# Optimization experiments

Hardware: AMD Instinct MI355X
Metric: run time of the kernel (lower is better)

The kernel has to match this reference:

```python
import jax, jax.numpy as jnp
import numpy as np

EMBED_DIM = 1024
NUM_HEADS = 16
HEAD_DIM = EMBED_DIM // NUM_HEADS


def layer_norm(x, gamma, beta, eps=1e-5):
    mu = jnp.mean(x, axis=-1, keepdims=True)
    var = jnp.var(x, axis=-1, keepdims=True)
    return (x - mu) * jax.lax.rsqrt(var + eps) * gamma + beta


def setup_inputs() -> dict:
    key = jax.random.key(0)
    ks = jax.random.split(key, 8)
    D = EMBED_DIM
    s = 1.0 / np.sqrt(D)
    x = jax.random.normal(ks[0], (2, 2048, D), dtype=jnp.float32)
    Wq = jax.random.uniform(ks[1], (D, D), jnp.float32, -s, s)
    Wk = jax.random.uniform(ks[2], (D, D), jnp.float32, -s, s)
    Wv = jax.random.uniform(ks[3], (D, D), jnp.float32, -s, s)
    W1 = jax.random.uniform(ks[4], (D, 4 * D), jnp.float32, -s, s)
    b1 = jnp.zeros((4 * D,), jnp.float32)
    W2 = jax.random.uniform(ks[5], (4 * D, D), jnp.float32, -1.0 / np.sqrt(4 * D), 1.0 / np.sqrt(4 * D))
    b2 = jnp.zeros((D,), jnp.float32)
    g1 = jnp.ones((D,), jnp.float32); be1 = jnp.zeros((D,), jnp.float32)
    g2 = jnp.ones((D,), jnp.float32); be2 = jnp.zeros((D,), jnp.float32)
    return {"x": x, "Wq": Wq, "Wk": Wk, "Wv": Wv, "W1": W1, "b1": b1,
            "W2": W2, "b2": b2, "g1": g1, "be1": be1, "g2": g2, "be2": be2}


def reference(x, Wq, Wk, Wv, W1, b1, W2, b2, g1, be1, g2, be2):
    B, S, D = x.shape
    H, Hd = NUM_HEADS, HEAD_DIM
    x_norm = layer_norm(x, g1, be1)
    # QKV projections (no bias), split into heads: [B, H, S, Hd]
    q = (x_norm @ Wq).reshape(B, S, H, Hd).transpose(0, 2, 1, 3)
    k = (x_norm @ Wk).reshape(B, S, H, Hd).transpose(0, 2, 1, 3)
    v = (x_norm @ Wv).reshape(B, S, H, Hd).transpose(0, 2, 1, 3)
    energy = jnp.einsum('bhqd,bhkd->bhqk', q, k)
    attn = jax.nn.softmax(energy / jnp.sqrt(jnp.float32(Hd)), axis=-1)
    out = jnp.einsum('bhqk,bhkd->bhqd', attn, v)
    attention = out.transpose(0, 2, 1, 3).reshape(B, S, D)
    x_res = attention + x
    x_norm2 = layer_norm(x_res, g2, be2)
    # Faithful quirk: FFN applied to x_res (not x_norm2)
    ffn_out = jax.nn.relu(x_res @ W1 + b1) @ W2 + b2
    return ffn_out + x_norm2
```

## Files before the change

kernel.cpp:

```cpp
#include <hip/hip_runtime.h>
#include <hip/hip_bf16.h>
#include <stdint.h>

typedef __hip_bfloat16 bf16;
typedef __attribute__((ext_vector_type(4))) float f32x4;
typedef __attribute__((ext_vector_type(8))) short s16x8;
typedef __attribute__((ext_vector_type(4))) short s16x4;

#define DEV static __device__ __forceinline__

DEV short f2bf(float f) {
  bf16 h = __float2bfloat16(f);
  short s;
  __builtin_memcpy(&s, &h, 2);
  return s;
}
DEV float bf2f(short s) {
  bf16 h;
  __builtin_memcpy(&h, &s, 2);
  return __bfloat162float(h);
}

__global__ __launch_bounds__(256) void transpose_cvt(
    const float* __restrict__ W, bf16* __restrict__ Wt, int K, int N)
{
  __shared__ float tile[32][33];
  const int n0 = blockIdx.x << 5;
  const int k0 = blockIdx.y << 5;
  const int tx = threadIdx.x & 31, ty = threadIdx.x >> 5;
#pragma unroll
  for (int i = 0; i < 4; ++i)
    tile[ty + i * 8][tx] = W[(size_t)(k0 + ty + i * 8) * N + n0 + tx];
  __syncthreads();
#pragma unroll
  for (int i = 0; i < 4; ++i)
    Wt[(size_t)(n0 + ty + i * 8) * K + k0 + tx] = __float2bfloat16(tile[tx][ty + i * 8]);
}

__global__ __launch_bounds__(256) void ln_bf16(
    const float* __restrict__ x, const float* __restrict__ g,
    const float* __restrict__ be, bf16* __restrict__ out)
{
  const int t = threadIdx.x;
  const size_t row = blockIdx.x;
  const float4 v = ((const float4*)(x + row * 1024))[t];
  float s = v.x + v.y + v.z + v.w;
  float ss = v.x * v.x + v.y * v.y + v.z * v.z + v.w * v.w;
#pragma unroll
  for (int off = 32; off > 0; off >>= 1) {
    s += __shfl_down(s, off);
    ss += __shfl_down(ss, off);
  }
  __shared__ float sh[8];
  const int wave = t >> 6, lane = t & 63;
  if (!lane) { sh[wave] = s; sh[4 + wave] = ss; }
  __syncthreads();
  s = sh[0] + sh[1] + sh[2] + sh[3];
  ss = sh[4] + sh[5] + sh[6] + sh[7];
  const float mean = s * (1.f / 1024.f);
  const float rstd = rsqrtf(ss * (1.f / 1024.f) - mean * mean + 1e-5f);
  const float4 gv = ((const float4*)g)[t];
  const float4 bv = ((const float4*)be)[t];
  s16x4 o;
  o[0] = f2bf((v.x - mean) * rstd * gv.x + bv.x);
  o[1] = f2bf((v.y - mean) * rstd * gv.y + bv.y);
  o[2] = f2bf((v.z - mean) * rstd * gv.z + bv.z);
  o[3] = f2bf((v.w - mean) * rstd * gv.w + bv.w);
  ((s16x4*)(out + row * 1024))[t] = o;
}

__global__ __launch_bounds__(256) void add_ln_bf16(
    const float* __restrict__ a, const float* __restrict__ x,
    const float* __restrict__ g, const float* __restrict__ be,
    bf16* __restrict__ xres, bf16* __restrict__ xnorm)
{
  const int t = threadIdx.x;
  const size_t row = blockIdx.x;
  const float4 av = ((const float4*)(a + row * 1024))[t];
  const float4 xv = ((const float4*)(x + row * 1024))[t];
  float4 v;
  v.x = av.x + xv.x; v.y = av.y + xv.y; v.z = av.z + xv.z; v.w = av.w + xv.w;
  float s = v.x + v.y + v.z + v.w;
  float ss = v.x * v.x + v.y * v.y + v.z * v.z + v.w * v.w;
#pragma unroll
  for (int off = 32; off > 0; off >>= 1) {
    s += __shfl_down(s, off);
    ss += __shfl_down(ss, off);
  }
  __shared__ float sh[8];
  const int wave = t >> 6, lane = t & 63;
  if (!lane) { sh[wave] = s; sh[4 + wave] = ss; }
  __syncthreads();
  s = sh[0] + sh[1] + sh[2] + sh[3];
  ss = sh[4] + sh[5] + sh[6] + sh[7];
  const float mean = s * (1.f / 1024.f);
  const float rstd = rsqrtf(ss * (1.f / 1024.f) - mean * mean + 1e-5f);
  const float4 gv = ((const float4*)g)[t];
  const float4 bv = ((const float4*)be)[t];
  s16x4 r, o;
  r[0] = f2bf(v.x); r[1] = f2bf(v.y); r[2] = f2bf(v.z); r[3] = f2bf(v.w);
  o[0] = f2bf((v.x - mean) * rstd * gv.x + bv.x);
  o[1] = f2bf((v.y - mean) * rstd * gv.y + bv.y);
  o[2] = f2bf((v.z - mean) * rstd * gv.z + bv.z);
  o[3] = f2bf((v.w - mean) * rstd * gv.w + bv.w);
  ((s16x4*)(xres + row * 1024))[t] = r;
  ((s16x4*)(xnorm + row * 1024))[t] = o;
}

template <int EPI>
__global__ __launch_bounds__(256) void gemm_bt(
    const bf16* __restrict__ A, const bf16* __restrict__ Bt,
    void* __restrict__ C, const float* __restrict__ bias,
    const bf16* __restrict__ add_bf16, int M, int N, int K)
{
  __shared__ bf16 sA0[128 * 64];
  __shared__ bf16 sB0[128 * 64];
  __shared__ bf16 sA1[128 * 64];
  __shared__ bf16 sB1[128 * 64];
  const int tid = threadIdx.x;
  const int wave = tid >> 6, lane = tid & 63;
  const int fr = lane & 15, fg = lane >> 4;
  const int f7 = fr & 7;
  const int wr = wave >> 1, wc = wave & 1;
  const int nbx = N >> 7;
  int bid = blockIdx.x;
  if ((gridDim.x & 7) == 0) {
    const int cpx = gridDim.x >> 3;
    bid = (bid & 7) * cpx + (bid >> 3);
  }
  const int brow = (bid / nbx) << 7;
  const int bcol = (bid % nbx) << 7;

  f32x4 acc[4][4] = {};

  const int rsub = lane >> 3;
  const int cl = (lane & 7) ^ rsub;
  size_t ga[4], gb[4];
  int la[4];
#pragma unroll
  for (int j = 0; j < 4; ++j) {
    const int r = wave * 32 + j * 8;
    ga[j] = (size_t)(brow + r + rsub) * K + cl * 8;
    gb[j] = (size_t)(bcol + r + rsub) * K + cl * 8;
    la[j] = r * 64;
  }

#define GSTAGE(SA, SB, koff)                                                   \
  do {                                                                         \
    _Pragma("unroll")                                                          \
    for (int jj = 0; jj < 4; ++jj) {                                           \
      __builtin_amdgcn_global_load_lds(                                        \
          (const __attribute__((address_space(1))) uint32_t*)(A + ga[jj] + (koff)), \
          (__attribute__((address_space(3))) uint32_t*)(&SA[la[jj]]), 16, 0, 0);  \
      __builtin_amdgcn_global_load_lds(                                        \
          (const __attribute__((address_space(1))) uint32_t*)(Bt + gb[jj] + (koff)),\
          (__attribute__((address_space(3))) uint32_t*)(&SB[la[jj]]), 16, 0, 0);  \
    }                                                                          \
  } while (0)

#define COMPUTE(SA, SB)                                                        \
  do {                                                                         \
    s16x8 af[4][2], bfr[4][2];                                                 \
    _Pragma("unroll")                                                          \
    for (int m = 0; m < 4; ++m)                                                \
      _Pragma("unroll")                                                        \
      for (int kk = 0; kk < 2; ++kk)                                           \
        af[m][kk] = *(const s16x8*)(&SA[(wr * 64 + m * 16 + fr) * 64 +         \
                                        (((kk * 4 + fg) ^ f7) << 3)]);         \
    _Pragma("unroll")                                                          \
    for (int n = 0; n < 4; ++n)                                                \
      _Pragma("unroll")                                                        \
      for (int kk = 0; kk < 2; ++kk)                                           \
        bfr[n][kk] = *(const s16x8*)(&SB[(wc * 64 + n * 16 + fr) * 64 +        \
                                         (((kk * 4 + fg) ^ f7) << 3)]);        \
    _Pragma("unroll")                                                          \
    for (int kk = 0; kk < 2; ++kk)                                             \
      _Pragma("unroll")                                                        \
      for (int m = 0; m < 4; ++m)                                              \
        _Pragma("unroll")                                                      \
        for (int n = 0; n < 4; ++n)                                            \
          acc[m][n] = __builtin_amdgcn_mfma_f32_16x16x32_bf16(                 \
              af[m][kk], bfr[n][kk], acc[m][n], 0, 0, 0);                      \
  } while (0)

  GSTAGE(sA0, sB0, 0);
  __syncthreads();

  int kt = 0;
  for (;;) {
    if (kt + 64 < K) {
      GSTAGE(sA1, sB1, kt + 64);
      COMPUTE(sA0, sB0);
      __syncthreads();
    } else {
      COMPUTE(sA0, sB0);
      break;
    }
    kt += 64;
    if (kt + 64 < K) {
      GSTAGE(sA0, sB0, kt + 64);
      COMPUTE(sA1, sB1);
      __syncthreads();
    } else {
      COMPUTE(sA1, sB1);
      break;
    }
    kt += 64;
  }
#undef GSTAGE
#undef COMPUTE

  const int crow = brow + wr * 64;
  const int ccol = bcol + wc * 64;
#pragma unroll
  for (int m = 0; m < 4; ++m) {
#pragma unroll
    for (int n = 0; n < 4; ++n) {
      const int col = ccol + n * 16 + fr;
#pragma unroll
      for (int j = 0; j < 4; ++j) {
        const int row = crow + m * 16 + fg * 4 + j;
        float v = acc[m][n][j];
        if (EPI == 0) {
          ((bf16*)C)[(size_t)row * N + col] = __float2bfloat16(v);
        } else if (EPI == 1) {
          v += bias[col];
          v = fmaxf(v, 0.f);
          ((bf16*)C)[(size_t)row * N + col] = __float2bfloat16(v);
        } else {
          float a;
          {
            bf16 hb = add_bf16[(size_t)row * N + col];
            a = __bfloat162float(hb);
          }
          ((float*)C)[(size_t)row * N + col] = v + bias[col] + a;
        }
      }
    }
  }
}

template <int EPI>
__global__ __launch_bounds__(512) void gemm256_bt(
    const bf16* __restrict__ A, const bf16* __restrict__ Bt,
    void* __restrict__ C, const float* __restrict__ bias, int M, int N, int K)
{
  __shared__ bf16 sA0[256 * 64];
  __shared__ bf16 sB0[256 * 64];
  __shared__ bf16 sA1[256 * 64];
  __shared__ bf16 sB1[256 * 64];
  const int tid = threadIdx.x;
  const int wave = tid >> 6, lane = tid & 63;
  const int fr = lane & 15, fg = lane >> 4;
  const int f7 = fr & 7;
  const int wr = wave >> 2, wc = wave & 3;
  const int nbx = N >> 8;
  int bid = blockIdx.x;
  if ((gridDim.x & 7) == 0) {
    const int cpx = gridDim.x >> 3;
    bid = (bid & 7) * cpx + (bid >> 3);
  }
  const int brow = (bid / nbx) << 8;
  const int bcol = (bid % nbx) << 8;

  f32x4 acc[8][4] = {};

  const int rsub = lane >> 3;
  const int cl = (lane & 7) ^ rsub;
  size_t ga[4], gb[4];
  int la[4];
#pragma unroll
  for (int j = 0; j < 4; ++j) {
    const int r = j * 64 + wave * 8;
    ga[j] = (size_t)(brow + r + rsub) * K + cl * 8;
    gb[j] = (size_t)(bcol + r + rsub) * K + cl * 8;
    la[j] = r * 64;
  }

#define STG6(SA, SB, koff)                                                     \
  do {                                                                         \
    _Pragma("unroll")                                                          \
    for (int jj = 0; jj < 4; ++jj) {                                           \
      __builtin_amdgcn_global_load_lds(                                        \
          (const __attribute__((address_space(1))) uint32_t*)(A + ga[jj] + (koff)), \
          (__attribute__((address_space(3))) uint32_t*)(&SA[la[jj]]), 16, 0, 0);  \
      __builtin_amdgcn_global_load_lds(                                        \
          (const __attribute__((address_space(1))) uint32_t*)(Bt + gb[jj] + (koff)),\
          (__attribute__((address_space(3))) uint32_t*)(&SB[la[jj]]), 16, 0, 0);  \
    }                                                                          \
  } while (0)

#define CMP6(SA, SB)                                                           \
  do {                                                                         \
    s16x8 bfr[4][2];                                                           \
    _Pragma("unroll")                                                          \
    for (int n = 0; n < 4; ++n)                                                \
      _Pragma("unroll")                                                        \
      for (int kk = 0; kk < 2; ++kk)                                           \
        bfr[n][kk] = *(const s16x8*)(&SB[(wc * 64 + n * 16 + fr) * 64 +        \
                                         (((kk * 4 + fg) ^ f7) << 3)]);        \
    __builtin_amdgcn_s_setprio(1);                                             \
    _Pragma("unroll")                                                          \
    for (int m = 0; m < 8; ++m) {                                              \
      s16x8 afm[2];                                                            \
      _Pragma("unroll")                                                        \
      for (int kk = 0; kk < 2; ++kk)                                           \
        afm[kk] = *(const s16x8*)(&SA[(wr * 128 + m * 16 + fr) * 64 +          \
                                      (((kk * 4 + fg) ^ f7) << 3)]);           \
      _Pragma("unroll")                                                        \
      for (int kk = 0; kk < 2; ++kk)                                           \
        _Pragma("unroll")                                                      \
        for (int n = 0; n < 4; ++n)                                            \
          acc[m][n] = __builtin_amdgcn_mfma_f32_16x16x32_bf16(                 \
              afm[kk], bfr[n][kk], acc[m][n], 0, 0, 0);                        \
    }                                                                          \
    __builtin_amdgcn_s_setprio(0);                                             \
  } while (0)

  STG6(sA0, sB0, 0);

  int kt = 0;
  for (;;) {
    if (kt + 64 < K) {
      STG6(sA1, sB1, kt + 64);
      asm volatile("s_waitcnt vmcnt(8)" ::: "memory");
    } else {
      asm volatile("s_waitcnt vmcnt(0)" ::: "memory");
    }
    __builtin_amdgcn_s_barrier();
    __builtin_amdgcn_sched_barrier(0);
    CMP6(sA0, sB0);
    if (kt + 64 >= K) break;
    __builtin_amdgcn_s_barrier();
    __builtin_amdgcn_sched_barrier(0);
    kt += 64;
    if (kt + 64 < K) {
      STG6(sA0, sB0, kt + 64);
      asm volatile("s_waitcnt vmcnt(8)" ::: "memory");
    } else {
      asm volatile("s_waitcnt vmcnt(0)" ::: "memory");
    }
    __builtin_amdgcn_s_barrier();
    __builtin_amdgcn_sched_barrier(0);
    CMP6(sA1, sB1);
    if (kt + 64 >= K) break;
    __builtin_amdgcn_s_barrier();
    __builtin_amdgcn_sched_barrier(0);
    kt += 64;
  }
#undef STG6
#undef CMP6

  const int crow = brow + wr * 128;
  const int ccol = bcol + wc * 64;
#pragma unroll
  for (int m = 0; m < 8; ++m) {
#pragma unroll
    for (int n = 0; n < 4; ++n) {
      const int col = ccol + n * 16 + fr;
#pragma unroll
      for (int j = 0; j < 4; ++j) {
        const int row = crow + m * 16 + fg * 4 + j;
        float v = acc[m][n][j];
        if (EPI == 0) {
          ((bf16*)C)[(size_t)row * N + col] = __float2bfloat16(v);
        } else {
          v += bias[col];
          v = fmaxf(v, 0.f);
          ((bf16*)C)[(size_t)row * N + col] = __float2bfloat16(v);
        }
      }
    }
  }
}

__global__ __launch_bounds__(512) void gemm256x128_bt(
    const bf16* __restrict__ A, const bf16* __restrict__ Bt,
    float* __restrict__ C, const float* __restrict__ bias,
    const bf16* __restrict__ add_bf16, int M, int N, int K)
{
  __shared__ bf16 sA0[256 * 64];
  __shared__ bf16 sB0[128 * 64];
  __shared__ bf16 sA1[256 * 64];
  __shared__ bf16 sB1[128 * 64];
  const int tid = threadIdx.x;
  const int wave = tid >> 6, lane = tid & 63;
  const int fr = lane & 15, fg = lane >> 4;
  const int f7 = fr & 7;
  const int wr = wave >> 1, wc = wave & 1;
  const int nbx = N >> 7;
  int bid = blockIdx.x;
  if ((gridDim.x & 7) == 0) {
    const int cpx = gridDim.x >> 3;
    bid = (bid & 7) * cpx + (bid >> 3);
  }
  const int brow = (bid / nbx) << 8;
  const int bcol = (bid % nbx) << 7;

  f32x4 acc[4][4] = {};

  const int rsub = lane >> 3;
  const int cl = (lane & 7) ^ rsub;
  size_t ga[4], gb[2];
  int laA[4], laB[2];
#pragma unroll
  for (int j = 0; j < 4; ++j) {
    const int r = j * 64 + wave * 8;
    ga[j] = (size_t)(brow + r + rsub) * K + cl * 8;
    laA[j] = r * 64;
  }
#pragma unroll
  for (int j = 0; j < 2; ++j) {
    const int r = j * 64 + wave * 8;
    gb[j] = (size_t)(bcol + r + rsub) * K + cl * 8;
    laB[j] = r * 64;
  }

#define STG7(SA, SB, koff)                                                     \
  do {                                                                         \
    _Pragma("unroll")                                                          \
    for (int jj = 0; jj < 4; ++jj)                                             \
      __builtin_amdgcn_global_load_lds(                                        \
          (const __attribute__((address_space(1))) uint32_t*)(A + ga[jj] + (koff)), \
          (__attribute__((address_space(3))) uint32_t*)(&SA[laA[jj]]), 16, 0, 0); \
    _Pragma("unroll")                                                          \
    for (int jj = 0; jj < 2; ++jj)                                             \
      __builtin_amdgcn_global_load_lds(                                        \
          (const __attribute__((address_space(1))) uint32_t*)(Bt + gb[jj] + (koff)),\
          (__attribute__((address_space(3))) uint32_t*)(&SB[laB[jj]]), 16, 0, 0); \
  } while (0)

#define CMP7(SA, SB)                                                           \
  do {                                                                         \
    s16x8 af[4][2], bfr[4][2];                                                 \
    _Pragma("unroll")                                                          \
    for (int m = 0; m < 4; ++m)                                                \
      _Pragma("unroll")                                                        \
      for (int kk = 0; kk < 2; ++kk)                                           \
        af[m][kk] = *(const s16x8*)(&SA[(wr * 64 + m * 16 + fr) * 64 +         \
                                        (((kk * 4 + fg) ^ f7) << 3)]);         \
    _Pragma("unroll")                                                          \
    for (int n = 0; n < 4; ++n)                                                \
      _Pragma("unroll")                                                        \
      for (int kk = 0; kk < 2; ++kk)                                           \
        bfr[n][kk] = *(const s16x8*)(&SB[(wc * 64 + n * 16 + fr) * 64 +        \
                                         (((kk * 4 + fg) ^ f7) << 3)]);        \
    __builtin_amdgcn_s_setprio(1);                                             \
    _Pragma("unroll")                                                          \
    for (int kk = 0; kk < 2; ++kk)                                             \
      _Pragma("unroll")                                                        \
      for (int m = 0; m < 4; ++m)                                              \
        _Pragma("unroll")                                                      \
        for (int n = 0; n < 4; ++n)                                            \
          acc[m][n] = __builtin_amdgcn_mfma_f32_16x16x32_bf16(                 \
              af[m][kk], bfr[n][kk], acc[m][n], 0, 0, 0);                      \
    __builtin_amdgcn_s_setprio(0);                                             \
  } while (0)

  STG7(sA0, sB0, 0);

  int kt = 0;
  for (;;) {
    if (kt + 64 < K) {
      STG7(sA1, sB1, kt + 64);
      asm volatile("s_waitcnt vmcnt(6)" ::: "memory");
    } else {
      asm volatile("s_waitcnt vmcnt(0)" ::: "memory");
    }
    __builtin_amdgcn_s_barrier();
    __builtin_amdgcn_sched_barrier(0);
    CMP7(sA0, sB0);
    if (kt + 64 >= K) break;
    __builtin_amdgcn_s_barrier();
    __builtin_amdgcn_sched_barrier(0);
    kt += 64;
    if (kt + 64 < K) {
      STG7(sA0, sB0, kt + 64);
      asm volatile("s_waitcnt vmcnt(6)" ::: "memory");
    } else {
      asm volatile("s_waitcnt vmcnt(0)" ::: "memory");
    }
    __builtin_amdgcn_s_barrier();
    __builtin_amdgcn_sched_barrier(0);
    CMP7(sA1, sB1);
    if (kt + 64 >= K) break;
    __builtin_amdgcn_s_barrier();
    __builtin_amdgcn_sched_barrier(0);
    kt += 64;
  }
#undef STG7
#undef CMP7

  const int crow = brow + wr * 64;
  const int ccol = bcol + wc * 64;
#pragma unroll
  for (int m = 0; m < 4; ++m) {
#pragma unroll
    for (int n = 0; n < 4; ++n) {
      const int col = ccol + n * 16 + fr;
#pragma unroll
      for (int j = 0; j < 4; ++j) {
        const int row = crow + m * 16 + fg * 4 + j;
        float a = __bfloat162float(add_bf16[(size_t)row * N + col]);
        C[(size_t)row * N + col] = acc[m][n][j] + bias[col] + a;
      }
    }
  }
}

__global__ __launch_bounds__(512, 4) void attn_fwd(
    const bf16* __restrict__ QK, const bf16* __restrict__ Vt,
    float* __restrict__ Out)
{
  const int LDK = 2048;
  const int qt = blockIdx.x;
  const int bh = blockIdx.y;
  const int b = bh >> 4, h = bh & 15;
  const int tid = threadIdx.x;
  const int wave = tid >> 6, lane = tid & 63;
  const int fr = lane & 15, fg = lane >> 4;
  const int f7 = fr & 7;

  const short* base = (const short*)QK + (size_t)b * 2048 * LDK;
  const short* Qp = base + h * 64;
  const short* Kp = base + 1024 + h * 64;
  const short* Vp = (const short*)Vt + (size_t)h * 64 * 4096 + b * 2048;
  const int q0 = qt * 128 + wave * 16;

  __shared__ short Kbuf0[64 * 64];
  __shared__ short Vbuf0[64 * 64];
  __shared__ short Kbuf1[64 * 64];
  __shared__ short Vbuf1[64 * 64];
  __shared__ short P_lds[8][16 * 72];
  short* Pw = P_lds[wave];

  const int rsub = lane >> 3;
  const int clog = (lane & 7) ^ rsub;
  const short* Ksrc = Kp + (size_t)(8 * wave + rsub) * LDK + clog * 8;
  const short* Vsrc = Vp + (size_t)(8 * wave + rsub) * 4096 + clog * 8;

  s16x8 qf0 = *(const s16x8*)(Qp + (size_t)(q0 + fr) * LDK + fg * 8);
  s16x8 qf1 = *(const s16x8*)(Qp + (size_t)(q0 + fr) * LDK + 32 + fg * 8);
#pragma unroll
  for (int i = 0; i < 8; ++i) {
    qf0[i] = f2bf(bf2f(qf0[i]) * 0.125f);
    qf1[i] = f2bf(bf2f(qf1[i]) * 0.125f);
  }

  f32x4 acc[4] = {};
  f32x4 mrow = {-1e30f, -1e30f, -1e30f, -1e30f};
  f32x4 lrow = {};

#define STAGE(KB, VB, koff)                                                    \
  do {                                                                         \
    __builtin_amdgcn_global_load_lds(                                          \
        (const __attribute__((address_space(1))) uint32_t*)(Ksrc + (size_t)(koff) * LDK), \
        (__attribute__((address_space(3))) uint32_t*)(&KB[wave * 512]),        \
        16, 0, 0);                                                             \
    __builtin_amdgcn_global_load_lds(                                          \
        (const __attribute__((address_space(1))) uint32_t*)(Vsrc + (koff)),    \
        (__attribute__((address_space(3))) uint32_t*)(&VB[wave * 512]),        \
        16, 0, 0);                                                             \
  } while (0)

#define ATTN_STEP(KB, VB)                                                      \
  do {                                                                         \
    f32x4 e[4];                                                                \
    __builtin_amdgcn_s_setprio(1);                                             \
    _Pragma("unroll")                                                          \
    for (int t = 0; t < 4; ++t) {                                              \
      const int ro = (t * 16 + fr) * 64;                                       \
      const s16x8 k0 = *(const s16x8*)(&KB[ro + ((fg ^ f7) << 3)]);            \
      const s16x8 k1 = *(const s16x8*)(&KB[ro + (((4 + fg) ^ f7) << 3)]);      \
      f32x4 z = {};                                                            \
      z = __builtin_amdgcn_mfma_f32_16x16x32_bf16(qf0, k0, z, 0, 0, 0);        \
      z = __builtin_amdgcn_mfma_f32_16x16x32_bf16(qf1, k1, z, 0, 0, 0);        \
      e[t] = z;                                                                \
    }                                                                          \
    __builtin_amdgcn_s_setprio(0);                                             \
    f32x4 lmx;                                                                 \
    _Pragma("unroll")                                                          \
    for (int j = 0; j < 4; ++j)                                                \
      lmx[j] = fmaxf(fmaxf(e[0][j], e[1][j]), fmaxf(e[2][j], e[3][j]));        \
    const bool need = (lmx[0] > mrow[0] + 8.f) | (lmx[1] > mrow[1] + 8.f) |    \
                      (lmx[2] > mrow[2] + 8.f) | (lmx[3] > mrow[3] + 8.f);     \
    if (__any(need)) {                                                         \
      f32x4 mx = lmx;                                                          \
      _Pragma("unroll")                                                        \
      for (int d = 1; d < 16; d <<= 1)                                         \
        _Pragma("unroll")                                                      \
        for (int j = 0; j < 4; ++j) mx[j] = fmaxf(mx[j], __shfl_xor(mx[j], d));\
      _Pragma("unroll")                                                        \
      for (int j = 0; j < 4; ++j) {                                            \
        const float mn = fmaxf(mrow[j], mx[j]);                                \
        const float al = __expf(mrow[j] - mn);                                 \
        lrow[j] *= al;                                                         \
        mrow[j] = mn;                                                          \
        _Pragma("unroll")                                                      \
        for (int nn = 0; nn < 4; ++nn) acc[nn][j] *= al;                       \
      }                                                                        \
    }                                                                          \
    _Pragma("unroll")                                                          \
    for (int j = 0; j < 4; ++j) {                                              \
      _Pragma("unroll")                                                        \
      for (int t = 0; t < 4; ++t) e[t][j] = __expf(e[t][j] - mrow[j]);         \
      lrow[j] += (e[0][j] + e[1][j]) + (e[2][j] + e[3][j]);                    \
    }                                                                          \
    _Pragma("unroll")                                                          \
    for (int t = 0; t < 4; ++t)                                                \
      _Pragma("unroll")                                                        \
      for (int j = 0; j < 4; ++j)                                              \
        Pw[(fg * 4 + j) * 72 + t * 16 + fr] = f2bf(e[t][j]);                   \
    const s16x8 pf0 = *(const s16x8*)(Pw + fr * 72 + fg * 8);                  \
    const s16x8 pf1 = *(const s16x8*)(Pw + fr * 72 + 32 + fg * 8);             \
    __builtin_amdgcn_s_setprio(1);                                             \
    _Pragma("unroll")                                                          \
    for (int nn = 0; nn < 4; ++nn) {                                           \
      const int ro = (nn * 16 + fr) * 64;                                      \
      const s16x8 vf0 = *(const s16x8*)(&VB[ro + ((fg ^ f7) << 3)]);           \
      const s16x8 vf1 = *(const s16x8*)(&VB[ro + (((4 + fg) ^ f7) << 3)]);     \
      acc[nn] = __builtin_amdgcn_mfma_f32_16x16x32_bf16(pf0, vf0, acc[nn], 0, 0, 0); \
      acc[nn] = __builtin_amdgcn_mfma_f32_16x16x32_bf16(pf1, vf1, acc[nn], 0, 0, 0); \
    }                                                                          \
    __builtin_amdgcn_s_setprio(0);                                             \
  } while (0)

  STAGE(Kbuf0, Vbuf0, 0);

  for (int kt = 0; kt < 2048; kt += 128) {
    STAGE(Kbuf1, Vbuf1, kt + 64);
    asm volatile("s_waitcnt vmcnt(2)" ::: "memory");
    __builtin_amdgcn_s_barrier();
    __builtin_amdgcn_sched_barrier(0);
    ATTN_STEP(Kbuf0, Vbuf0);
    __builtin_amdgcn_s_barrier();
    __builtin_amdgcn_sched_barrier(0);
    if (kt + 128 < 2048) {
      STAGE(Kbuf0, Vbuf0, kt + 128);
      asm volatile("s_waitcnt vmcnt(2)" ::: "memory");
    } else {
      asm volatile("s_waitcnt vmcnt(0)" ::: "memory");
    }
    __builtin_amdgcn_s_barrier();
    __builtin_amdgcn_sched_barrier(0);
    ATTN_STEP(Kbuf1, Vbuf1);
    __builtin_amdgcn_s_barrier();
    __builtin_amdgcn_sched_barrier(0);
  }
#undef STAGE
#undef ATTN_STEP

#pragma unroll
  for (int d = 1; d < 16; d <<= 1)
#pragma unroll
    for (int j = 0; j < 4; ++j) lrow[j] += __shfl_xor(lrow[j], d);
  f32x4 inv;
#pragma unroll
  for (int j = 0; j < 4; ++j) inv[j] = 1.0f / lrow[j];
  float* outp = Out + (size_t)(b * 2048 + q0) * 1024 + h * 64;
#pragma unroll
  for (int nn = 0; nn < 4; ++nn)
#pragma unroll
    for (int j = 0; j < 4; ++j)
      outp[(size_t)(fg * 4 + j) * 1024 + nn * 16 + fr] = acc[nn][j] * inv[j];
}

extern "C" void kernel_launch(void* const* d_in, const int* in_sizes, int n_in,
                              void* d_out, int out_size, void* d_ws, size_t ws_size,
                              hipStream_t stream)
{
  const float* x   = (const float*)d_in[0];
  const float* Wq  = (const float*)d_in[1];
  const float* Wk  = (const float*)d_in[2];
  const float* Wv  = (const float*)d_in[3];
  const float* W1  = (const float*)d_in[4];
  const float* b1  = (const float*)d_in[5];
  const float* W2  = (const float*)d_in[6];
  const float* b2  = (const float*)d_in[7];
  const float* g1  = (const float*)d_in[8];
  const float* be1 = (const float*)d_in[9];
  const float* g2  = (const float*)d_in[10];
  const float* be2 = (const float*)d_in[11];
  float* out = (float*)d_out;

  const int M = 4096, D = 1024, DF = 4096;

  bf16* Wqk_t = (bf16*)d_ws;
  bf16* Wv_t  = Wqk_t + (size_t)2048 * 1024;
  bf16* W1t   = Wv_t + (size_t)1024 * 1024;
  bf16* W2t   = W1t + (size_t)4096 * 1024;
  bf16* big   = W2t + (size_t)4096 * 1024;
  bf16* QK    = big;
  bf16* Vt    = big + (size_t)8 * 1024 * 1024;
  bf16* hbuf  = big;
  char* p2    = (char*)(big + (size_t)16 * 1024 * 1024);
  bf16* xnorm = (bf16*)p2;
  float* attnO = (float*)p2;
  char* p3    = p2 + (size_t)M * D * sizeof(float);
  bf16* xres  = (bf16*)p3;
  bf16* xnorm2 = xres + (size_t)M * D;

  transpose_cvt<<<dim3(32, 32), 256, 0, stream>>>(Wq, Wqk_t, D, D);
  transpose_cvt<<<dim3(32, 32), 256, 0, stream>>>(Wk, Wqk_t + (size_t)D * D, D, D);
  transpose_cvt<<<dim3(32, 32), 256, 0, stream>>>(Wv, Wv_t, D, D);
  transpose_cvt<<<dim3(128, 32), 256, 0, stream>>>(W1, W1t, D, DF);
  transpose_cvt<<<dim3(32, 128), 256, 0, stream>>>(W2, W2t, DF, D);
  ln_bf16<<<M, 256, 0, stream>>>(x, g1, be1, xnorm);
  gemm_bt<0><<<(M / 128) * (2048 / 128), 256, 0, stream>>>(
      xnorm, Wqk_t, QK, nullptr, nullptr, M, 2048, D);
  gemm_bt<0><<<(D / 128) * (M / 128), 256, 0, stream>>>(
      Wv_t, xnorm, Vt, nullptr, nullptr, D, M, D);
  attn_fwd<<<dim3(16, 32), 512, 0, stream>>>(QK, Vt, attnO);
  add_ln_bf16<<<M, 256, 0, stream>>>(attnO, x, g2, be2, xres, xnorm2);
  gemm256_bt<1><<<(M / 256) * (DF / 256), 512, 0, stream>>>(
      xres, W1t, hbuf, b1, M, DF, D);
  gemm256x128_bt<<<(M / 256) * (D / 128), 512, 0, stream>>>(
      hbuf, W2t, out, b2, xnorm2, M, D, DF);
}
```

Before: 247.5 us.

## Split-K the second FFN GEMM with separate epilogue reduction kernel

```diff
diff --git a/kernel.cpp b/kernel.cpp
--- a/kernel.cpp
+++ b/kernel.cpp
@@ -107,6 +107,24 @@
   ((s16x4*)(xnorm + row * 1024))[t] = o;
 }
 
+__global__ __launch_bounds__(256) void ffn2_epi(
+    const float* __restrict__ p0, float* __restrict__ out,
+    const float* __restrict__ bias, const bf16* __restrict__ xn2)
+{
+  const int t = threadIdx.x;
+  const size_t row = blockIdx.x;
+  const float4 a = ((const float4*)(p0 + row * 1024))[t];
+  const float4 b = ((const float4*)(out + row * 1024))[t];
+  const float4 bv = ((const float4*)bias)[t];
+  const s16x4 xv = ((const s16x4*)(xn2 + row * 1024))[t];
+  float4 o;
+  o.x = a.x + b.x + bv.x + bf2f(xv[0]);
+  o.y = a.y + b.y + bv.y + bf2f(xv[1]);
+  o.z = a.z + b.z + bv.z + bf2f(xv[2]);
+  o.w = a.w + b.w + bv.w + bf2f(xv[3]);
+  ((float4*)(out + row * 1024))[t] = o;
+}
+
 template <int EPI>
 __global__ __launch_bounds__(256) void gemm_bt(
     const bf16* __restrict__ A, const bf16* __restrict__ Bt,
@@ -240,6 +258,125 @@
   }
 }
 
+__global__ __launch_bounds__(256) void gemm_splitk(
+    const bf16* __restrict__ A, const bf16* __restrict__ Bt,
+    float* __restrict__ P0, float* __restrict__ P1, int M, int N, int K, int KH)
+{
+  __shared__ bf16 sA0[128 * 64];
+  __shared__ bf16 sB0[128 * 64];
+  __shared__ bf16 sA1[128 * 64];
+  __shared__ bf16 sB1[128 * 64];
+  const int tid = threadIdx.x;
+  const int wave = tid >> 6, lane = tid & 63;
+  const int fr = lane & 15, fg = lane >> 4;
+  const int f7 = fr & 7;
+  const int wr = wave >> 1, wc = wave & 1;
+  const int nbx = N >> 7;
+  int bid = blockIdx.x;
+  if ((gridDim.x & 7) == 0) {
+    const int cpx = gridDim.x >> 3;
+    bid = (bid & 7) * cpx + (bid >> 3);
+  }
+  const int brow = (bid / nbx) << 7;
+  const int bcol = (bid % nbx) << 7;
+  const int kbeg = blockIdx.y * KH;
+  float* Cp = blockIdx.y ? P1 : P0;
+
+  f32x4 acc[4][4] = {};
+
+  const int rsub = lane >> 3;
+  const int cl = (lane & 7) ^ rsub;
+  size_t ga[4], gb[4];
+  int la[4];
+#pragma unroll
+  for (int j = 0; j < 4; ++j) {
+    const int r = wave * 32 + j * 8;
+    ga[j] = (size_t)(brow + r + rsub) * K + cl * 8 + kbeg;
+    gb[j] = (size_t)(bcol + r + rsub) * K + cl * 8 + kbeg;
+    la[j] = r * 64;
+  }
+
+#define GSTAGE(SA, SB, koff)                                                   \
+  do {                                                                         \
+    _Pragma("unroll")                                                          \
+    for (int jj = 0; jj < 4; ++jj) {                                           \
+      __builtin_amdgcn_global_load_lds(                                        \
+          (const __attribute__((address_space(1))) uint32_t*)(A + ga[jj] + (koff)), \
+          (__attribute__((address_space(3))) uint32_t*)(&SA[la[jj]]), 16, 0, 0);  \
+      __builtin_amdgcn_global_load_lds(                                        \
+          (const __attribute__((address_space(1))) uint32_t*)(Bt + gb[jj] + (koff)),\
+          (__attribute__((address_space(3))) uint32_t*)(&SB[la[jj]]), 16, 0, 0);  \
+    }                                                                          \
+  } while (0)
+
+#define COMPUTE(SA, SB)                                                        \
+  do {                                                                         \
+    s16x8 af[4][2], bfr[4][2];                                                 \
+    _Pragma("unroll")                                                          \
+    for (int m = 0; m < 4; ++m)                                                \
+      _Pragma("unroll")                                                        \
+      for (int kk = 0; kk < 2; ++kk)                                           \
+        af[m][kk] = *(const s16x8*)(&SA[(wr * 64 + m * 16 + fr) * 64 +         \
+                                        (((kk * 4 + fg) ^ f7) << 3)]);         \
+    _Pragma("unroll")                                                          \
+    for (int n = 0; n < 4; ++n)                                                \
+      _Pragma("unroll")                                                        \
+      for (int kk = 0; kk < 2; ++kk)                                           \
+        bfr[n][kk] = *(const s16x8*)(&SB[(wc * 64 + n * 16 + fr) * 64 +        \
+                                         (((kk * 4 + fg) ^ f7) << 3)]);        \
+    _Pragma("unroll")                                                          \
+    for (int kk = 0; kk < 2; ++kk)                                             \
+      _Pragma("unroll")                                                        \
+      for (int m = 0; m < 4; ++m)                                              \
+        _Pragma("unroll")                                                      \
+        for (int n = 0; n < 4; ++n)                                            \
+          acc[m][n] = __builtin_amdgcn_mfma_f32_16x16x32_bf16(                 \
+              af[m][kk], bfr[n][kk], acc[m][n], 0, 0, 0);                      \
+  } while (0)
+
+  GSTAGE(sA0, sB0, 0);
+  __syncthreads();
+
+  int kt = 0;
+  for (;;) {
+    if (kt + 64 < KH) {
+      GSTAGE(sA1, sB1, kt + 64);
+      COMPUTE(sA0, sB0);
+      __syncthreads();
+    } else {
+      COMPUTE(sA0, sB0);
+      break;
+    }
+    kt += 64;
+    if (kt + 64 < KH) {
+      GSTAGE(sA0, sB0, kt + 64);
+      COMPUTE(sA1, sB1);
+      __syncthreads();
+    } else {
+      COMPUTE(sA1, sB1);
+      break;
+    }
+    kt += 64;
+  }
+#undef GSTAGE
+#undef COMPUTE
+
+  const int crow = brow + wr * 64;
+  const int ccol = bcol + wc * 64;
+#pragma unroll
+  for (int m = 0; m < 4; ++m) {
+#pragma unroll
+    for (int n = 0; n < 4; ++n) {
+      const int col = ccol + n * 16 + fr;
+#pragma unroll
+      for (int j = 0; j < 4; ++j) {
+        const int row = crow + m * 16 + fg * 4 + j;
+        Cp[(size_t)row * N + col] = acc[m][n][j];
+      }
+    }
+  }
+}
+
 template <int EPI>
 __global__ __launch_bounds__(512) void gemm256_bt(
     const bf16* __restrict__ A, const bf16* __restrict__ Bt,
@@ -374,140 +511,6 @@
   }
 }
 
-__global__ __launch_bounds__(512) void gemm256x128_bt(
-    const bf16* __restrict__ A, const bf16* __restrict__ Bt,
-    float* __restrict__ C, const float* __restrict__ bias,
-    const bf16* __restrict__ add_bf16, int M, int N, int K)
-{
-  __shared__ bf16 sA0[256 * 64];
-  __shared__ bf16 sB0[128 * 64];
-  __shared__ bf16 sA1[256 * 64];
-  __shared__ bf16 sB1[128 * 64];
-  const int tid = threadIdx.x;
-  const int wave = tid >> 6, lane = tid & 63;
-  const int fr = lane & 15, fg = lane >> 4;
-  const int f7 = fr & 7;
-  const int wr = wave >> 1, wc = wave & 1;
-  const int nbx = N >> 7;
-  int bid = blockIdx.x;
-  if ((gridDim.x & 7) == 0) {
-    const int cpx = gridDim.x >> 3;
-    bid = (bid & 7) * cpx + (bid >> 3);
-  }
-  const int brow = (bid / nbx) << 8;
-  const int bcol = (bid % nbx) << 7;
-
-  f32x4 acc[4][4] = {};
-
-  const int rsub = lane >> 3;
-  const int cl = (lane & 7) ^ rsub;
-  size_t ga[4], gb[2];
-  int laA[4], laB[2];
-#pragma unroll
-  for (int j = 0; j < 4; ++j) {
-    const int r = j * 64 + wave * 8;
-    ga[j] = (size_t)(brow + r + rsub) * K + cl * 8;
-    laA[j] = r * 64;
-  }
-#pragma unroll
-  for (int j = 0; j < 2; ++j) {
-    const int r = j * 64 + wave * 8;
-    gb[j] = (size_t)(bcol + r + rsub) * K + cl * 8;
-    laB[j] = r * 64;
-  }
-
-#define STG7(SA, SB, koff)                                                     \
-  do {                                                                         \
-    _Pragma("unroll")                                                          \
-    for (int jj = 0; jj < 4; ++jj)                                             \
-      __builtin_amdgcn_global_load_lds(                                        \
-          (const __attribute__((address_space(1))) uint32_t*)(A + ga[jj] + (koff)), \
-          (__attribute__((address_space(3))) uint32_t*)(&SA[laA[jj]]), 16, 0, 0); \
-    _Pragma("unroll")                                                          \
-    for (int jj = 0; jj < 2; ++jj)                                             \
-      __builtin_amdgcn_global_load_lds(                                        \
-          (const __attribute__((address_space(1))) uint32_t*)(Bt + gb[jj] + (koff)),\
-          (__attribute__((address_space(3))) uint32_t*)(&SB[laB[jj]]), 16, 0, 0); \
-  } while (0)
-
-#define CMP7(SA, SB)                                                           \
-  do {                                                                         \
-    s16x8 af[4][2], bfr[4][2];                                                 \
-    _Pragma("unroll")                                                          \
-    for (int m = 0; m < 4; ++m)                                                \
-      _Pragma("unroll")                                                        \
-      for (int kk = 0; kk < 2; ++kk)                                           \
-        af[m][kk] = *(const s16x8*)(&SA[(wr * 64 + m * 16 + fr) * 64 +         \
-                                        (((kk * 4 + fg) ^ f7) << 3)]);         \
-    _Pragma("unroll")                                                          \
-    for (int n = 0; n < 4; ++n)                                                \
-      _Pragma("unroll")                                                        \
-      for (int kk = 0; kk < 2; ++kk)                                           \
-        bfr[n][kk] = *(const s16x8*)(&SB[(wc * 64 + n * 16 + fr) * 64 +        \
-                                         (((kk * 4 + fg) ^ f7) << 3)]);        \
-    __builtin_amdgcn_s_setprio(1);                                             \
-    _Pragma("unroll")                                                          \
-    for (int kk = 0; kk < 2; ++kk)                                             \
-      _Pragma("unroll")                                                        \
-      for (int m = 0; m < 4; ++m)                                              \
-        _Pragma("unroll")                                                      \
-        for (int n = 0; n < 4; ++n)                                            \
-          acc[m][n] = __builtin_amdgcn_mfma_f32_16x16x32_bf16(                 \
-              af[m][kk], bfr[n][kk], acc[m][n], 0, 0, 0);                      \
-    __builtin_amdgcn_s_setprio(0);                                             \
-  } while (0)
-
-  STG7(sA0, sB0, 0);
-
-  int kt = 0;
-  for (;;) {
-    if (kt + 64 < K) {
-      STG7(sA1, sB1, kt + 64);
-      asm volatile("s_waitcnt vmcnt(6)" ::: "memory");
-    } else {
-      asm volatile("s_waitcnt vmcnt(0)" ::: "memory");
-    }
-    __builtin_amdgcn_s_barrier();
-    __builtin_amdgcn_sched_barrier(0);
-    CMP7(sA0, sB0);
-    if (kt + 64 >= K) break;
-    __builtin_amdgcn_s_barrier();
-    __builtin_amdgcn_sched_barrier(0);
-    kt += 64;
-    if (kt + 64 < K) {
-      STG7(sA0, sB0, kt + 64);
-      asm volatile("s_waitcnt vmcnt(6)" ::: "memory");
-    } else {
-      asm volatile("s_waitcnt vmcnt(0)" ::: "memory");
-    }
-    __builtin_amdgcn_s_barrier();
-    __builtin_amdgcn_sched_barrier(0);
-    CMP7(sA1, sB1);
-    if (kt + 64 >= K) break;
-    __builtin_amdgcn_s_barrier();
-    __builtin_amdgcn_sched_barrier(0);
-    kt += 64;
-  }
-#undef STG7
-#undef CMP7
-
-  const int crow = brow + wr * 64;
-  const int ccol = bcol + wc * 64;
-#pragma unroll
-  for (int m = 0; m < 4; ++m) {
-#pragma unroll
-    for (int n = 0; n < 4; ++n) {
-      const int col = ccol + n * 16 + fr;
-#pragma unroll
-      for (int j = 0; j < 4; ++j) {
-        const int row = crow + m * 16 + fg * 4 + j;
-        float a = __bfloat162float(add_bf16[(size_t)row * N + col]);
-        C[(size_t)row * N + col] = acc[m][n][j] + bias[col] + a;
-      }
-    }
-  }
-}
-
 __global__ __launch_bounds__(512, 4) void attn_fwd(
     const bf16* __restrict__ QK, const bf16* __restrict__ Vt,
     float* __restrict__ Out)
@@ -696,6 +699,7 @@
   char* p2    = (char*)(big + (size_t)16 * 1024 * 1024);
   bf16* xnorm = (bf16*)p2;
   float* attnO = (float*)p2;
+  float* part0 = (float*)p2;
   char* p3    = p2 + (size_t)M * D * sizeof(float);
   bf16* xres  = (bf16*)p3;
   bf16* xnorm2 = xres + (size_t)M * D;
@@ -714,6 +718,7 @@
   add_ln_bf16<<<M, 256, 0, stream>>>(attnO, x, g2, be2, xres, xnorm2);
   gemm256_bt<1><<<(M / 256) * (DF / 256), 512, 0, stream>>>(
       xres, W1t, hbuf, b1, M, DF, D);
-  gemm256x128_bt<<<(M / 256) * (D / 128), 512, 0, stream>>>(
-      hbuf, W2t, out, b2, xnorm2, M, D, DF);
-}
+  gemm_splitk<<<dim3((M / 128) * (D / 128), 2), 256, 0, stream>>>(
+      hbuf, W2t, part0, out, M, D, DF, DF / 2);
+  ffn2_epi<<<M, 256, 0, stream>>>(part0, out, b2, xnorm2);
+}
```

Result: faster. 227.1 us (-8.2%).
